# Performance work log

Measured on AMD Instinct MI355X. Metric: run time of the kernel, lower is better.

Reference implementation:

```python
import jax, jax.numpy as jnp
import numpy as np

R = 0.4          # ball radius
K = 32           # max_neighbors
S = 512          # cluster_num
BN_EPS = 1e-5


def fps(data, npoint):
    """Furthest point sampling. data: [B,N,C] -> idx [B,npoint] int32.
    Deterministic start at index 0 (original uses randint)."""
    B, N, C = data.shape

    def step(carry, _):
        dist, far = carry
        cent = jnp.take_along_axis(data, far[:, None, None], axis=1)  # [B,1,C]
        d = jnp.sum((data - cent) ** 2, -1)                           # [B,N]
        dist = jnp.minimum(dist, d)
        new_far = jnp.argmax(dist, -1).astype(jnp.int32)
        return (dist, new_far), far

    dist0 = jnp.full((B, N), 1e10, data.dtype)
    far0 = jnp.zeros((B,), jnp.int32)
    _, idxs = jax.lax.scan(step, (dist0, far0), None, length=npoint)
    return idxs.T  # [B,npoint]


def gather_points(data, idx):
    """data [B,N,C], idx [B,S] -> [B,S,C]"""
    return jnp.take_along_axis(data, idx[..., None], axis=1)


def gather_groups(data, idx):
    """data [B,N,C], idx [B,S,K] -> [B,S,K,C]"""
    B, N, C = data.shape
    _, Sq, Kq = idx.shape
    flat = jnp.take_along_axis(data, idx.reshape(B, Sq * Kq)[..., None], axis=1)
    return flat.reshape(B, Sq, Kq, C)


def square_dist(a, b):
    """a [B,N,C], b [B,M,C] -> [B,N,M]"""
    return (-2.0 * jnp.einsum('bnc,bmc->bnm', a, b)
            + jnp.sum(a ** 2, -1)[:, :, None]
            + jnp.sum(b ** 2, -1)[:, None, :])


def knn_query(data, query, max_neighbors, r):
    """Ball query: indices of up to max_neighbors points within r, padded with
    the first valid index. data [B,N,C], query [B,S,C] -> [B,S,K] int32."""
    B, N, _ = data.shape
    d = square_dist(query, data)                              # [B,S,N]
    idx = jnp.where(d <= r * r, jnp.arange(N, dtype=jnp.int32)[None, None, :], N)
    idx = jnp.sort(idx, axis=-1)[:, :, :max_neighbors]        # ascending, N = invalid
    first = idx[:, :, :1]
    return jnp.where(idx == N, first, idx)


def mlp_layer(x, w, b, g, be):
    """1x1 Conv2d + BatchNorm2d (training-mode batch stats) + ReLU.
    x [B,S,K,Cin], w [Cout,Cin] -> [B,S,K,Cout]"""
    y = jnp.einsum('bskc,oc->bsko', x, w) + b
    m = jnp.mean(y, axis=(0, 1, 2))
    v = jnp.var(y, axis=(0, 1, 2))
    y = (y - m) * jax.lax.rsqrt(v + BN_EPS) * g + be
    return jax.nn.relu(y)


def setup_inputs() -> dict:
    key = jax.random.key(0)
    ks = jax.random.split(key, 5)
    B, N = 16, 8192
    data = jax.random.normal(ks[0], (B, N, 3), jnp.float32)
    data_feature = jax.random.normal(ks[1], (B, N, 3), jnp.float32)
    w0 = jax.random.normal(ks[2], (64, 6), jnp.float32) * 0.1
    w1 = jax.random.normal(ks[3], (64, 64), jnp.float32) * 0.1
    w2 = jax.random.normal(ks[4], (128, 64), jnp.float32) * 0.1
    zeros = lambda c: jnp.zeros((c,), jnp.float32)
    ones = lambda c: jnp.ones((c,), jnp.float32)
    return dict(data=data, data_feature=data_feature,
                w0=w0, b0=zeros(64), g0=ones(64), be0=zeros(64),
                w1=w1, b1=zeros(64), g1=ones(64), be1=zeros(64),
                w2=w2, b2=zeros(128), g2=ones(128), be2=zeros(128))


def reference(data, data_feature, w0, b0, g0, be0, w1, b1, g1, be1, w2, b2, g2, be2):
    B, N, C = data.shape
    fps_idx = fps(data, S)                              # [B,S]
    centroids = gather_points(data, fps_idx)            # [B,S,3]
    nbr_idx = knn_query(data, centroids, K, R)          # [B,S,K]
    sample = gather_groups(data, nbr_idx)               # [B,S,K,3]
    sample_norm = sample - centroids[:, :, None, :]
    feat = gather_groups(data_feature, nbr_idx)         # [B,S,K,3]
    x = jnp.concatenate([sample_norm, feat], axis=-1)   # [B,S,K,6]
    x = mlp_layer(x, w0, b0, g0, be0)
    x = mlp_layer(x, w1, b1, g1, be1)
    x = mlp_layer(x, w2, b2, g2, be2)
    out = jnp.max(x, axis=2)                            # [B,S,128]
    return centroids, out
```

## Files before the change

### kernel.cpp

```cpp
#include <hip/hip_runtime.h>
#include <math.h>

constexpr int Bc = 16;
constexpr int Nc = 8192;
constexpr int Sc = 512;
constexpr int Kc = 32;
constexpr int Pc = Bc * Sc * Kc;

constexpr int NBALL_BLK = 240;
constexpr int NBALL_WAVES = NBALL_BLK * 4;

typedef float v2f __attribute__((ext_vector_type(2)));

#if defined(__has_builtin)
#if __has_builtin(__builtin_elementwise_fma)
#define PKFMA(a, b, c) __builtin_elementwise_fma(a, b, c)
#endif
#endif
#ifndef PKFMA
__device__ __forceinline__ v2f pkfma_(v2f a, v2f b, v2f c) {
  v2f r; r.x = fmaf(a.x, b.x, c.x); r.y = fmaf(a.y, b.y, c.y); return r;
}
#define PKFMA(a, b, c) pkfma_(a, b, c)
#endif

template <int CTRL>
__device__ __forceinline__ float dpp_max_stage(float x) {
  int p = __builtin_amdgcn_update_dpp(0, __float_as_int(x), CTRL, 0xf, 0xf, true);
  return fmaxf(x, __int_as_float(p));
}

__global__ __launch_bounds__(256, 1)
void fps_ball_fused(const float* __restrict__ data,
                    const float* __restrict__ feat,
                    const float* __restrict__ w0,
                    const float* __restrict__ b0,
                    int* __restrict__ idx_pub,
                    float* __restrict__ cent_out,
                    float* __restrict__ x0,
                    float* __restrict__ part0) {
  __shared__ float lx[Nc], ly[Nc], lz[Nc];
  __shared__ unsigned long long red_k[2][4];
  __shared__ int idx_hist[Sc];
  __shared__ int nbr[4][Kc];
  __shared__ float x0s[4][6][Kc];

  const int t = threadIdx.x;
  const int lane = t & 63, w = t >> 6;

  if (blockIdx.x < Bc) {
    const int b = blockIdx.x;
    const float* db = data + (size_t)b * Nc * 3;

    float px[32], py[32], pz[32], dist[32];
#pragma unroll
    for (int j = 0; j < 32; ++j) {
      int p = t + 256 * j;
      px[j] = db[p * 3 + 0];
      py[j] = db[p * 3 + 1];
      pz[j] = db[p * 3 + 2];
      dist[j] = 1e10f;
      lx[p] = px[j]; ly[p] = py[j]; lz[p] = pz[j];
    }
    __syncthreads();

    int far = 0;
    for (int it = 0; it < Sc; ++it) {
      const int sfar = __builtin_amdgcn_readfirstlane(far);
      if (t == 0) {
        idx_hist[it] = sfar;
        atomicExch(&idx_pub[(b << 9) + it], sfar);
      }
      const float cx = lx[sfar];
      const float cy = ly[sfar];
      const float cz = lz[sfar];

      float best = -1.0f; int bj = 0;
#pragma unroll
      for (int j = 0; j < 32; ++j) {
        float dx = __fsub_rn(px[j], cx);
        float dy = __fsub_rn(py[j], cy);
        float dz = __fsub_rn(pz[j], cz);
        float d = __fadd_rn(__fadd_rn(__fmul_rn(dx, dx), __fmul_rn(dy, dy)),
                            __fmul_rn(dz, dz));
        float nd = fminf(dist[j], d);
        dist[j] = nd;
        if (nd > best) { best = nd; bj = j; }
      }
      const int bidx = t + 256 * bj;

      float wmax = best;
      wmax = dpp_max_stage<0xB1>(wmax);
      wmax = dpp_max_stage<0x4E>(wmax);
      wmax = dpp_max_stage<0x141>(wmax);
      wmax = dpp_max_stage<0x140>(wmax);
      wmax = fmaxf(wmax, __shfl_xor(wmax, 16));
      wmax = fmaxf(wmax, __shfl_xor(wmax, 32));

      unsigned long long m = __ballot(best == wmax);
      int idx;
      if (__popcll(m) == 1) {
        idx = __shfl(bidx, (int)__ffsll((long long)m) - 1);
      } else {
        int cand = (best == wmax) ? bidx : 0x7fffffff;
#pragma unroll
        for (int off = 32; off; off >>= 1) cand = min(cand, __shfl_xor(cand, off));
        idx = cand;
      }

      unsigned long long key =
          ((unsigned long long)__float_as_uint(wmax) << 32) |
          (unsigned long long)(0xFFFFFFFFu - (unsigned)idx);
      const int par = it & 1;
      if (lane == 0) red_k[par][w] = key;
      __syncthreads();

      unsigned long long k0 = red_k[par][0];
      unsigned long long k1 = red_k[par][1];
      unsigned long long k2 = red_k[par][2];
      unsigned long long k3 = red_k[par][3];
      unsigned long long ka = (k0 > k1) ? k0 : k1;
      unsigned long long kb = (k2 > k3) ? k2 : k3;
      unsigned long long kk = (ka > kb) ? ka : kb;
      far = (int)(0xFFFFFFFFu - (unsigned)(kk & 0xFFFFFFFFull));
    }

    __syncthreads();
    for (int s = t; s < Sc; s += 256) {
      int id = idx_hist[s];
      size_t o = ((size_t)b * Sc + s) * 3;
      cent_out[o + 0] = lx[id];
      cent_out[o + 1] = ly[id];
      cent_out[o + 2] = lz[id];
    }
  } else {
    const int wid = (blockIdx.x - Bc) * 4 + w;
    const int bb = wid & 15;
    const int u  = wid >> 4;
    const float* db = data + (size_t)bb * Nc * 3;
    const float* fb = feat + (size_t)bb * Nc * 3;

    float W[6];
#pragma unroll
    for (int c = 0; c < 6; ++c) W[c] = w0[lane * 6 + c];
    const float bias = b0[lane];
    float sum = 0.f, sq = 0.f;

    for (int s = u; s < Sc; s += 60) {
      const int q = bb * Sc + s;

      float px = db[lane * 3 + 0];
      float py = db[lane * 3 + 1];
      float pz = db[lane * 3 + 2];

      int ci;
      for (;;) {
        int t0 = -1;
        if (lane == 0) t0 = atomicAdd(&idx_pub[q], 0);
        ci = __shfl(t0, 0);
        if (ci >= 0) break;
        __builtin_amdgcn_s_sleep(32);
      }

      const float qx = db[ci * 3 + 0];
      const float qy = db[ci * 3 + 1];
      const float qz = db[ci * 3 + 2];
      const float q2 = __fadd_rn(__fadd_rn(__fmul_rn(qx, qx), __fmul_rn(qy, qy)),
                                 __fmul_rn(qz, qz));

      int have = 0;
      for (int base = 0; base < Nc; base += 64) {
        const int inext = (base + 64 + lane) & (Nc - 1);
        float nx = db[inext * 3 + 0];
        float ny = db[inext * 3 + 1];
        float nz = db[inext * 3 + 2];

        float p2 = __fadd_rn(__fadd_rn(__fmul_rn(px, px), __fmul_rn(py, py)),
                             __fmul_rn(pz, pz));
        float dt = fmaf(qz, pz, fmaf(qy, py, __fmul_rn(qx, px)));
        float d = __fadd_rn(__fadd_rn(__fmul_rn(-2.0f, dt), q2), p2);
        bool ok = d <= 0.16f;
        unsigned long long mask = __ballot(ok);
        if (mask) {
          int pos = have + __popcll(mask & ((1ull << lane) - 1ull));
          if (ok && pos < Kc) nbr[w][pos] = base + lane;
          have += __popcll(mask);
          if (have >= Kc) break;
        }
        px = nx; py = ny; pz = nz;
      }
      if (have > Kc) have = Kc;

      if (lane < Kc) {
        int j = nbr[w][lane < have ? lane : 0];
        float sx = __fsub_rn(db[j * 3 + 0], qx);
        float sy = __fsub_rn(db[j * 3 + 1], qy);
        float sz = __fsub_rn(db[j * 3 + 2], qz);
        float fx = fb[j * 3 + 0], fy = fb[j * 3 + 1], fz = fb[j * 3 + 2];
        size_t pidx = (size_t)q * Kc + lane;
        x0[(size_t)0 * Pc + pidx] = sx;
        x0[(size_t)1 * Pc + pidx] = sy;
        x0[(size_t)2 * Pc + pidx] = sz;
        x0[(size_t)3 * Pc + pidx] = fx;
        x0[(size_t)4 * Pc + pidx] = fy;
        x0[(size_t)5 * Pc + pidx] = fz;
        x0s[w][0][lane] = sx; x0s[w][1][lane] = sy; x0s[w][2][lane] = sz;
        x0s[w][3][lane] = fx; x0s[w][4][lane] = fy; x0s[w][5][lane] = fz;
      }

#pragma unroll 4
      for (int k = 0; k < Kc; ++k) {
        float y = bias;
#pragma unroll
        for (int c = 0; c < 6; ++c) y = fmaf(x0s[w][c][k], W[c], y);
        sum += y;
        sq = fmaf(y, y, sq);
      }
    }
    part0[(size_t)wid * 128 + lane] = sum;
    part0[(size_t)wid * 128 + 64 + lane] = sq;
  }
}

__global__ __launch_bounds__(256)
void reduce_k(const float* __restrict__ part, int nblk, int nch,
              const float* __restrict__ g, const float* __restrict__ be,
              float* __restrict__ AB) {
  const int o = blockIdx.x;
  const int t = threadIdx.x;
  double sum = 0.0, sq = 0.0;
  for (int i = t; i < nblk; i += 256) {
    sum += (double)part[(size_t)i * (2 * nch) + o];
    sq  += (double)part[(size_t)i * (2 * nch) + nch + o];
  }
  __shared__ double ls[256], lq[256];
  ls[t] = sum; lq[t] = sq;
  __syncthreads();
  for (int s = 128; s > 0; s >>= 1) {
    if (t < s) { ls[t] += ls[t + s]; lq[t] += lq[t + s]; }
    __syncthreads();
  }
  if (t == 0) {
    double m = ls[0] / (double)Pc;
    double v = lq[0] / (double)Pc - m * m;
    double A = (double)g[o] / sqrt(v + 1e-5);
    AB[o] = (float)A;
    AB[nch + o] = (float)((double)be[o] - m * A);
  }
}

__global__ __launch_bounds__(256)
void reduce2_final_k(const float* __restrict__ part, int nblk,
                     const float* __restrict__ g, const float* __restrict__ be,
                     const float* __restrict__ maxy2,
                     float* __restrict__ out) {
  const int o = blockIdx.x;
  const int t = threadIdx.x;
  double sum = 0.0, sq = 0.0;
  for (int i = t; i < nblk; i += 256) {
    sum += (double)part[(size_t)i * 256 + o];
    sq  += (double)part[(size_t)i * 256 + 128 + o];
  }
  __shared__ double ls[256], lq[256];
  ls[t] = sum; lq[t] = sq;
  __syncthreads();
  for (int s = 128; s > 0; s >>= 1) {
    if (t < s) { ls[t] += ls[t + s]; lq[t] += lq[t + s]; }
    __syncthreads();
  }
  __shared__ float sA, sB;
  if (t == 0) {
    double m = ls[0] / (double)Pc;
    double v = lq[0] / (double)Pc - m * m;
    double A = (double)g[o] / sqrt(v + 1e-5);
    sA = (float)A;
    sB = (float)((double)be[o] - m * A);
  }
  __syncthreads();
  const float A = sA, B = sB;
  for (int grp = t; grp < Bc * Sc; grp += 256) {
    float v = maxy2[(size_t)grp * 128 + o];
    out[(size_t)grp * 128 + o] = fmaxf(fmaf(v, A, B), 0.f);
  }
}

__global__ __launch_bounds__(256, 1)
void pass_b(const float* __restrict__ x0, const float* __restrict__ w0,
            const float* __restrict__ b0, const float* __restrict__ AB0,
            const float* __restrict__ w1, const float* __restrict__ b1,
            float* __restrict__ y1) {
  const int p = blockIdx.x * 256 + threadIdx.x;

  float xin[6];
#pragma unroll
  for (int c = 0; c < 6; ++c) xin[c] = x0[(size_t)c * Pc + p];

  v2f x1p[32];
#pragma unroll
  for (int j = 0; j < 32; ++j) {
    float y0v = b0[2 * j];
#pragma unroll
    for (int c = 0; c < 6; ++c) y0v = fmaf(xin[c], w0[(2 * j) * 6 + c], y0v);
    x1p[j].x = fmaxf(fmaf(y0v, AB0[2 * j], AB0[64 + 2 * j]), 0.f);
    float y1v = b0[2 * j + 1];
#pragma unroll
    for (int c = 0; c < 6; ++c) y1v = fmaf(xin[c], w0[(2 * j + 1) * 6 + c], y1v);
    x1p[j].y = fmaxf(fmaf(y1v, AB0[2 * j + 1], AB0[64 + 2 * j + 1]), 0.f);
  }

  const v2f* __restrict__ w1v = (const v2f*)w1;

  for (int o = 0; o < 64; ++o) {
    v2f a01; a01.x = b1[o]; a01.y = 0.f;
    v2f a23; a23.x = 0.f;   a23.y = 0.f;
#pragma unroll
    for (int c2 = 0; c2 < 32; c2 += 2) {
      a01 = PKFMA(x1p[c2 + 0], w1v[o * 32 + c2 + 0], a01);
      a23 = PKFMA(x1p[c2 + 1], w1v[o * 32 + c2 + 1], a23);
    }
    y1[(size_t)o * Pc + p] = (a01.x + a01.y) + (a23.x + a23.y);
  }
}

__global__ __launch_bounds__(256)
void stats1_k(const float* __restrict__ y1, float* __restrict__ pair1) {
  const int b = blockIdx.x;
  const int o = b >> 4, seg = b & 15;
  const int t = threadIdx.x;
  const float* plane = y1 + (size_t)o * Pc + (size_t)seg * 16384;
  float sum = 0.f, sq = 0.f;
  for (int i = t; i < 16384; i += 256) {
    float v = plane[i];
    sum += v;
    sq = fmaf(v, v, sq);
  }
  __shared__ float ls[256], lq[256];
  ls[t] = sum; lq[t] = sq;
  __syncthreads();
  for (int s = 128; s > 0; s >>= 1) {
    if (t < s) { ls[t] += ls[t + s]; lq[t] += lq[t + s]; }
    __syncthreads();
  }
  if (t == 0) {
    pair1[(size_t)b * 2 + 0] = ls[0];
    pair1[(size_t)b * 2 + 1] = lq[0];
  }
}

__global__ __launch_bounds__(64)
void reduceAB_pairs_k(const float* __restrict__ pair, int nseg,
                      const float* __restrict__ g, const float* __restrict__ be,
                      float* __restrict__ AB, int nch) {
  const int o = blockIdx.x;
  if (threadIdx.x == 0) {
    double sum = 0.0, sq = 0.0;
    for (int s = 0; s < nseg; ++s) {
      sum += (double)pair[(size_t)(o * nseg + s) * 2 + 0];
      sq  += (double)pair[(size_t)(o * nseg + s) * 2 + 1];
    }
    double m = sum / (double)Pc;
    double v = sq / (double)Pc - m * m;
    double A = (double)g[o] / sqrt(v + 1e-5);
    AB[o] = (float)A;
    AB[nch + o] = (float)((double)be[o] - m * A);
  }
}

__global__ __launch_bounds__(256, 1)
void pass_c(const float* __restrict__ y1, const float* __restrict__ AB1,
            const float* __restrict__ w2, const float* __restrict__ b2,
            float* __restrict__ maxy2, float* __restrict__ part2) {
  const int p = blockIdx.x * 256 + threadIdx.x;
  const int lane = threadIdx.x & 63, w = threadIdx.x >> 6;
  const int grp = p >> 5;

  v2f x2p[32];
#pragma unroll
  for (int c = 0; c < 64; c += 2) {
    float v0 = y1[(size_t)c * Pc + p];
    float v1 = y1[(size_t)(c + 1) * Pc + p];
    x2p[c >> 1].x = fmaxf(fmaf(v0, AB1[c], AB1[64 + c]), 0.f);
    x2p[c >> 1].y = fmaxf(fmaf(v1, AB1[c + 1], AB1[64 + c + 1]), 0.f);
  }

  const v2f* __restrict__ w2v = (const v2f*)w2;

  __shared__ float ssum[4][128][9], ssq[4][128][9];

  for (int o = 0; o < 128; ++o) {
    v2f a01; a01.x = b2[o]; a01.y = 0.f;
    v2f a23; a23.x = 0.f;   a23.y = 0.f;
#pragma unroll
    for (int c2 = 0; c2 < 32; c2 += 2) {
      a01 = PKFMA(x2p[c2 + 0], w2v[o * 32 + c2 + 0], a01);
      a23 = PKFMA(x2p[c2 + 1], w2v[o * 32 + c2 + 1], a23);
    }
    float acc = (a01.x + a01.y) + (a23.x + a23.y);

    float mx = acc;
#pragma unroll
    for (int off = 16; off > 0; off >>= 1) mx = fmaxf(mx, __shfl_xor(mx, off));
    if ((lane & 31) == 0) maxy2[(size_t)grp * 128 + o] = mx;

    float sv = acc + __shfl_xor(acc, 1);
    sv += __shfl_xor(sv, 2);
    sv += __shfl_xor(sv, 4);
    float q = acc * acc;
    float qv = q + __shfl_xor(q, 1);
    qv += __shfl_xor(qv, 2);
    qv += __shfl_xor(qv, 4);
    if ((lane & 7) == 0) {
      ssum[w][o][lane >> 3] = sv;
      ssq[w][o][lane >> 3] = qv;
    }
  }
  __syncthreads();
  {
    const int o = threadIdx.x & 127;
    const bool isq = threadIdx.x >= 128;
    float s = 0.f;
#pragma unroll
    for (int ww = 0; ww < 4; ++ww)
      for (int k = 0; k < 8; ++k)
        s += isq ? ssq[ww][o][k] : ssum[ww][o][k];
    part2[blockIdx.x * 256 + threadIdx.x] = s;
  }
}

extern "C" void kernel_launch(void* const* d_in, const int* in_sizes, int n_in,
                              void* d_out, int out_size, void* d_ws, size_t ws_size,
                              hipStream_t stream) {
  const float* data = (const float*)d_in[0];
  const float* feat = (const float*)d_in[1];
  const float* w0 = (const float*)d_in[2];
  const float* b0 = (const float*)d_in[3];
  const float* g0 = (const float*)d_in[4];
  const float* be0 = (const float*)d_in[5];
  const float* w1 = (const float*)d_in[6];
  const float* b1 = (const float*)d_in[7];
  const float* g1 = (const float*)d_in[8];
  const float* be1 = (const float*)d_in[9];
  const float* w2 = (const float*)d_in[10];
  const float* b2 = (const float*)d_in[11];
  const float* g2 = (const float*)d_in[12];
  const float* be2 = (const float*)d_in[13];
  float* out = (float*)d_out;

  float* ws = (float*)d_ws;
  int* idx_pub = (int*)ws; ws += (size_t)Bc * Sc;
  float* x0 = ws;      ws += (size_t)6 * Pc;
  float* y1 = ws;      ws += (size_t)64 * Pc;
  float* maxy2 = ws;   ws += (size_t)Bc * Sc * 128;
  float* part0 = ws;   ws += (size_t)NBALL_WAVES * 128;
  float* pair1 = ws;   ws += 1024 * 2;
  float* part2 = ws;   ws += 1024 * 256;
  float* AB0 = ws;     ws += 128;
  float* AB1 = ws;     ws += 128;

  hipMemsetAsync(idx_pub, 0xFF, (size_t)Bc * Sc * sizeof(int), stream);

  fps_ball_fused<<<Bc + NBALL_BLK, 256, 0, stream>>>(data, feat, w0, b0,
                                                     idx_pub, out, x0, part0);
  reduce_k<<<64, 256, 0, stream>>>(part0, NBALL_WAVES, 64, g0, be0, AB0);
  pass_b<<<Pc / 256, 256, 0, stream>>>(x0, w0, b0, AB0, w1, b1, y1);
  stats1_k<<<1024, 256, 0, stream>>>(y1, pair1);
  reduceAB_pairs_k<<<64, 64, 0, stream>>>(pair1, 16, g1, be1, AB1, 64);
  pass_c<<<Pc / 256, 256, 0, stream>>>(y1, AB1, w2, b2, maxy2, part2);
  reduce2_final_k<<<128, 256, 0, stream>>>(part2, 1024, g2, be2, maxy2,
                                           out + (size_t)Bc * Sc * 3);
}
```

Baseline: 786.7 us.

## Register-block pass_b and pass_c over two points and two output channels

Each thread in pass_b and pass_c now handles two points and two output channels per iteration, so every weight load feeds four packed FMAs instead of one. Grid size is halved, and part2 and the final reduce are resized to match. Each wave starts its output-channel loop at a different offset, which spreads weight accesses across waves. The cost is roughly double the register use, which may cut occupancy or cause spills, and half as many blocks to fill the GPU.

```diff
diff --git a/kernel.cpp b/kernel.cpp
--- a/kernel.cpp
+++ b/kernel.cpp
@@ -289,36 +289,70 @@
             const float* __restrict__ b0, const float* __restrict__ AB0,
             const float* __restrict__ w1, const float* __restrict__ b1,
             float* __restrict__ y1) {
-  const int p = blockIdx.x * 256 + threadIdx.x;
-
-  float xin[6];
-#pragma unroll
-  for (int c = 0; c < 6; ++c) xin[c] = x0[(size_t)c * Pc + p];
-
-  v2f x1p[32];
+  const int t = threadIdx.x;
+  const int w = t >> 6;
+  const int p0 = blockIdx.x * 512 + t;
+  const int p1 = p0 + 256;
+
+  float xinA[6], xinB[6];
+#pragma unroll
+  for (int c = 0; c < 6; ++c) {
+    xinA[c] = x0[(size_t)c * Pc + p0];
+    xinB[c] = x0[(size_t)c * Pc + p1];
+  }
+
+  v2f x1pA[32], x1pB[32];
 #pragma unroll
   for (int j = 0; j < 32; ++j) {
-    float y0v = b0[2 * j];
-#pragma unroll
-    for (int c = 0; c < 6; ++c) y0v = fmaf(xin[c], w0[(2 * j) * 6 + c], y0v);
-    x1p[j].x = fmaxf(fmaf(y0v, AB0[2 * j], AB0[64 + 2 * j]), 0.f);
-    float y1v = b0[2 * j + 1];
-#pragma unroll
-    for (int c = 0; c < 6; ++c) y1v = fmaf(xin[c], w0[(2 * j + 1) * 6 + c], y1v);
-    x1p[j].y = fmaxf(fmaf(y1v, AB0[2 * j + 1], AB0[64 + 2 * j + 1]), 0.f);
+    float ya0 = b0[2 * j];
+#pragma unroll
+    for (int c = 0; c < 6; ++c) ya0 = fmaf(xinA[c], w0[(2 * j) * 6 + c], ya0);
+    x1pA[j].x = fmaxf(fmaf(ya0, AB0[2 * j], AB0[64 + 2 * j]), 0.f);
+    float ya1 = b0[2 * j + 1];
+#pragma unroll
+    for (int c = 0; c < 6; ++c) ya1 = fmaf(xinA[c], w0[(2 * j + 1) * 6 + c], ya1);
+    x1pA[j].y = fmaxf(fmaf(ya1, AB0[2 * j + 1], AB0[64 + 2 * j + 1]), 0.f);
+    float yb0 = b0[2 * j];
+#pragma unroll
+    for (int c = 0; c < 6; ++c) yb0 = fmaf(xinB[c], w0[(2 * j) * 6 + c], yb0);
+    x1pB[j].x = fmaxf(fmaf(yb0, AB0[2 * j], AB0[64 + 2 * j]), 0.f);
+    float yb1 = b0[2 * j + 1];
+#pragma unroll
+    for (int c = 0; c < 6; ++c) yb1 = fmaf(xinB[c], w0[(2 * j + 1) * 6 + c], yb1);
+    x1pB[j].y = fmaxf(fmaf(yb1, AB0[2 * j + 1], AB0[64 + 2 * j + 1]), 0.f);
   }
 
   const v2f* __restrict__ w1v = (const v2f*)w1;
 
-  for (int o = 0; o < 64; ++o) {
-    v2f a01; a01.x = b1[o]; a01.y = 0.f;
-    v2f a23; a23.x = 0.f;   a23.y = 0.f;
+  for (int oi = 0; oi < 64; oi += 2) {
+    const int o = (oi + (w << 4)) & 63;
+    v2f aA01; aA01.x = b1[o];     aA01.y = 0.f;
+    v2f aA23; aA23.x = 0.f;       aA23.y = 0.f;
+    v2f cA01; cA01.x = b1[o + 1]; cA01.y = 0.f;
+    v2f cA23; cA23.x = 0.f;       cA23.y = 0.f;
+    v2f aB01; aB01.x = b1[o];     aB01.y = 0.f;
+    v2f aB23; aB23.x = 0.f;       aB23.y = 0.f;
+    v2f cB01; cB01.x = b1[o + 1]; cB01.y = 0.f;
+    v2f cB23; cB23.x = 0.f;       cB23.y = 0.f;
 #pragma unroll
     for (int c2 = 0; c2 < 32; c2 += 2) {
-      a01 = PKFMA(x1p[c2 + 0], w1v[o * 32 + c2 + 0], a01);
-      a23 = PKFMA(x1p[c2 + 1], w1v[o * 32 + c2 + 1], a23);
-    }
-    y1[(size_t)o * Pc + p] = (a01.x + a01.y) + (a23.x + a23.y);
+      v2f wa0 = w1v[o * 32 + c2 + 0];
+      v2f wa1 = w1v[o * 32 + c2 + 1];
+      v2f wc0 = w1v[(o + 1) * 32 + c2 + 0];
+      v2f wc1 = w1v[(o + 1) * 32 + c2 + 1];
+      aA01 = PKFMA(x1pA[c2 + 0], wa0, aA01);
+      aA23 = PKFMA(x1pA[c2 + 1], wa1, aA23);
+      cA01 = PKFMA(x1pA[c2 + 0], wc0, cA01);
+      cA23 = PKFMA(x1pA[c2 + 1], wc1, cA23);
+      aB01 = PKFMA(x1pB[c2 + 0], wa0, aB01);
+      aB23 = PKFMA(x1pB[c2 + 1], wa1, aB23);
+      cB01 = PKFMA(x1pB[c2 + 0], wc0, cB01);
+      cB23 = PKFMA(x1pB[c2 + 1], wc1, cB23);
+    }
+    y1[(size_t)o * Pc + p0]       = (aA01.x + aA01.y) + (aA23.x + aA23.y);
+    y1[(size_t)o * Pc + p1]       = (aB01.x + aB01.y) + (aB23.x + aB23.y);
+    y1[(size_t)(o + 1) * Pc + p0] = (cA01.x + cA01.y) + (cA23.x + cA23.y);
+    y1[(size_t)(o + 1) * Pc + p1] = (cB01.x + cB01.y) + (cB23.x + cB23.y);
   }
 }
 
@@ -370,48 +404,123 @@
 void pass_c(const float* __restrict__ y1, const float* __restrict__ AB1,
             const float* __restrict__ w2, const float* __restrict__ b2,
             float* __restrict__ maxy2, float* __restrict__ part2) {
-  const int p = blockIdx.x * 256 + threadIdx.x;
-  const int lane = threadIdx.x & 63, w = threadIdx.x >> 6;
-  const int grp = p >> 5;
-
-  v2f x2p[32];
+  const int t = threadIdx.x;
+  const int lane = t & 63, w = t >> 6;
+  const int p0 = blockIdx.x * 512 + t;
+  const int p1 = p0 + 256;
+  const int grp0 = p0 >> 5, grp1 = p1 >> 5;
+
+  v2f x2pA[32], x2pB[32];
 #pragma unroll
   for (int c = 0; c < 64; c += 2) {
-    float v0 = y1[(size_t)c * Pc + p];
-    float v1 = y1[(size_t)(c + 1) * Pc + p];
-    x2p[c >> 1].x = fmaxf(fmaf(v0, AB1[c], AB1[64 + c]), 0.f);
-    x2p[c >> 1].y = fmaxf(fmaf(v1, AB1[c + 1], AB1[64 + c + 1]), 0.f);
+    float vA0 = y1[(size_t)c * Pc + p0];
+    float vA1 = y1[(size_t)(c + 1) * Pc + p0];
+    x2pA[c >> 1].x = fmaxf(fmaf(vA0, AB1[c], AB1[64 + c]), 0.f);
+    x2pA[c >> 1].y = fmaxf(fmaf(vA1, AB1[c + 1], AB1[64 + c + 1]), 0.f);
+    float vB0 = y1[(size_t)c * Pc + p1];
+    float vB1 = y1[(size_t)(c + 1) * Pc + p1];
+    x2pB[c >> 1].x = fmaxf(fmaf(vB0, AB1[c], AB1[64 + c]), 0.f);
+    x2pB[c >> 1].y = fmaxf(fmaf(vB1, AB1[c + 1], AB1[64 + c + 1]), 0.f);
   }
 
   const v2f* __restrict__ w2v = (const v2f*)w2;
 
   __shared__ float ssum[4][128][9], ssq[4][128][9];
 
-  for (int o = 0; o < 128; ++o) {
-    v2f a01; a01.x = b2[o]; a01.y = 0.f;
-    v2f a23; a23.x = 0.f;   a23.y = 0.f;
+  for (int oi = 0; oi < 128; oi += 2) {
+    const int o = (oi + (w << 5)) & 127;
+    v2f aA01; aA01.x = b2[o];     aA01.y = 0.f;
+    v2f aA23; aA23.x = 0.f;       aA23.y = 0.f;
+    v2f cA01; cA01.x = b2[o + 1]; cA01.y = 0.f;
+    v2f cA23; cA23.x = 0.f;       cA23.y = 0.f;
+    v2f aB01; aB01.x = b2[o];     aB01.y = 0.f;
+    v2f aB23; aB23.x = 0.f;       aB23.y = 0.f;
+    v2f cB01; cB01.x = b2[o + 1]; cB01.y = 0.f;
+    v2f cB23; cB23.x = 0.f;       cB23.y = 0.f;
 #pragma unroll
     for (int c2 = 0; c2 < 32; c2 += 2) {
-      a01 = PKFMA(x2p[c2 + 0], w2v[o * 32 + c2 + 0], a01);
-      a23 = PKFMA(x2p[c2 + 1], w2v[o * 32 + c2 + 1], a23);
-    }
-    float acc = (a01.x + a01.y) + (a23.x + a23.y);
-
-    float mx = acc;
-#pragma unroll
-    for (int off = 16; off > 0; off >>= 1) mx = fmaxf(mx, __shfl_xor(mx, off));
-    if ((lane & 31) == 0) maxy2[(size_t)grp * 128 + o] = mx;
-
-    float sv = acc + __shfl_xor(acc, 1);
-    sv += __shfl_xor(sv, 2);
-    sv += __shfl_xor(sv, 4);
-    float q = acc * acc;
-    float qv = q + __shfl_xor(q, 1);
-    qv += __shfl_xor(qv, 2);
-    qv += __shfl_xor(qv, 4);
-    if ((lane & 7) == 0) {
-      ssum[w][o][lane >> 3] = sv;
-      ssq[w][o][lane >> 3] = qv;
+      v2f wa0 = w2v[o * 32 + c2 + 0];
+      v2f wa1 = w2v[o * 32 + c2 + 1];
+      v2f wc0 = w2v[(o + 1) * 32 + c2 + 0];
+      v2f wc1 = w2v[(o + 1) * 32 + c2 + 1];
+      aA01 = PKFMA(x2pA[c2 + 0], wa0, aA01);
+      aA23 = PKFMA(x2pA[c2 + 1], wa1, aA23);
+      cA01 = PKFMA(x2pA[c2 + 0], wc0, cA01);
+      cA23 = PKFMA(x2pA[c2 + 1], wc1, cA23);
+      aB01 = PKFMA(x2pB[c2 + 0], wa0, aB01);
+      aB23 = PKFMA(x2pB[c2 + 1], wa1, aB23);
+      cB01 = PKFMA(x2pB[c2 + 0], wc0, cB01);
+      cB23 = PKFMA(x2pB[c2 + 1], wc1, cB23);
+    }
+    float accA0 = (aA01.x + aA01.y) + (aA23.x + aA23.y);
+    float accA1 = (cA01.x + cA01.y) + (cA23.x + cA23.y);
+    float accB0 = (aB01.x + aB01.y) + (aB23.x + aB23.y);
+    float accB1 = (cB01.x + cB01.y) + (cB23.x + cB23.y);
+
+    {
+      float mx = accA0;
+#pragma unroll
+      for (int off = 16; off > 0; off >>= 1) mx = fmaxf(mx, __shfl_xor(mx, off));
+      if ((lane & 31) == 0) maxy2[(size_t)grp0 * 128 + o] = mx;
+    }
+    {
+      float mx = accA1;
+#pragma unroll
+      for (int off = 16; off > 0; off >>= 1) mx = fmaxf(mx, __shfl_xor(mx, off));
+      if ((lane & 31) == 0) maxy2[(size_t)grp0 * 128 + o + 1] = mx;
+    }
+    {
+      float mx = accB0;
+#pragma unroll
+      for (int off = 16; off > 0; off >>= 1) mx = fmaxf(mx, __shfl_xor(mx, off));
+      if ((lane & 31) == 0) maxy2[(size_t)grp1 * 128 + o] = mx;
+    }
+    {
+      float mx = accB1;
+#pragma unroll
+      for (int off = 16; off > 0; off >>= 1) mx = fmaxf(mx, __shfl_xor(mx, off));
+      if ((lane & 31) == 0) maxy2[(size_t)grp1 * 128 + o + 1] = mx;
+    }
+
+    {
+      float sv = accA0 + __shfl_xor(accA0, 1);
+      sv += __shfl_xor(sv, 2);
+      sv += __shfl_xor(sv, 4);
+      float sw = accB0 + __shfl_xor(accB0, 1);
+      sw += __shfl_xor(sw, 2);
+      sw += __shfl_xor(sw, 4);
+      float q = accA0 * accA0;
+      float qv = q + __shfl_xor(q, 1);
+      qv += __shfl_xor(qv, 2);
+      qv += __shfl_xor(qv, 4);
+      float r = accB0 * accB0;
+      float qw = r + __shfl_xor(r, 1);
+      qw += __shfl_xor(qw, 2);
+      qw += __shfl_xor(qw, 4);
+      if ((lane & 7) == 0) {
+        ssum[w][o][lane >> 3] = sv + sw;
+        ssq[w][o][lane >> 3] = qv + qw;
+      }
+    }
+    {
+      float sv = accA1 + __shfl_xor(accA1, 1);
+      sv += __shfl_xor(sv, 2);
+      sv += __shfl_xor(sv, 4);
+      float sw = accB1 + __shfl_xor(accB1, 1);
+      sw += __shfl_xor(sw, 2);
+      sw += __shfl_xor(sw, 4);
+      float q = accA1 * accA1;
+      float qv = q + __shfl_xor(q, 1);
+      qv += __shfl_xor(qv, 2);
+      qv += __shfl_xor(qv, 4);
+      float r = accB1 * accB1;
+      float qw = r + __shfl_xor(r, 1);
+      qw += __shfl_xor(qw, 2);
+      qw += __shfl_xor(qw, 4);
+      if ((lane & 7) == 0) {
+        ssum[w][o + 1][lane >> 3] = sv + sw;
+        ssq[w][o + 1][lane >> 3] = qv + qw;
+      }
     }
   }
   __syncthreads();
@@ -453,7 +562,7 @@
   float* maxy2 = ws;   ws += (size_t)Bc * Sc * 128;
   float* part0 = ws;   ws += (size_t)NBALL_WAVES * 128;
   float* pair1 = ws;   ws += 1024 * 2;
-  float* part2 = ws;   ws += 1024 * 256;
+  float* part2 = ws;   ws += 512 * 256;
   float* AB0 = ws;     ws += 128;
   float* AB1 = ws;     ws += 128;
 
@@ -462,10 +571,10 @@
   fps_ball_fused<<<Bc + NBALL_BLK, 256, 0, stream>>>(data, feat, w0, b0,
                                                      idx_pub, out, x0, part0);
   reduce_k<<<64, 256, 0, stream>>>(part0, NBALL_WAVES, 64, g0, be0, AB0);
-  pass_b<<<Pc / 256, 256, 0, stream>>>(x0, w0, b0, AB0, w1, b1, y1);
+  pass_b<<<Pc / 512, 256, 0, stream>>>(x0, w0, b0, AB0, w1, b1, y1);
   stats1_k<<<1024, 256, 0, stream>>>(y1, pair1);
   reduceAB_pairs_k<<<64, 64, 0, stream>>>(pair1, 16, g1, be1, AB1, 64);
-  pass_c<<<Pc / 256, 256, 0, stream>>>(y1, AB1, w2, b2, maxy2, part2);
-  reduce2_final_k<<<128, 256, 0, stream>>>(part2, 1024, g2, be2, maxy2,
+  pass_c<<<Pc / 512, 256, 0, stream>>>(y1, AB1, w2, b2, maxy2, part2);
+  reduce2_final_k<<<128, 256, 0, stream>>>(part2, 512, g2, be2, maxy2,
                                            out + (size_t)Bc * Sc * 3);
 }
```

Measured after the change: 842.8 us. 7.1% more time.
